# Kernel optimization log

Measured on AMD Instinct MI355X. Metric: run time of the kernel, lower is better.

Reference implementation:

```python
import jax, jax.numpy as jnp
import numpy as np

DIM = 128
NUM_HEADS = 16
DPH = DIM // NUM_HEADS
N_ATOMS = 50000
N_EDGES = 400000
LN_EPS = 1e-5


def setup_inputs() -> dict:
    key = jax.random.key(0)
    ks = jax.random.split(key, 12)
    inp = {
        "node_feat": jax.random.normal(ks[0], (N_ATOMS, DIM), jnp.float32),
        "edge_feat": jax.random.normal(ks[1], (N_EDGES, NUM_HEADS, DPH), jnp.float32),
        "edge_vec": jax.random.normal(ks[2], (N_EDGES, 3, 1, 1), jnp.float32),
        "radial": jax.random.uniform(ks[3], (N_EDGES,), jnp.float32),
        "qkv_w": jax.random.normal(ks[4], (DIM, 3 * DIM), jnp.float32) / np.sqrt(DIM),
        "qkv_b": jnp.zeros((3 * DIM,), jnp.float32),
        "out_w": jax.random.normal(ks[5], (DIM, DIM), jnp.float32) / np.sqrt(DIM),
        "out_b": jnp.zeros((DIM,), jnp.float32),
        "ln_g": jnp.ones((DIM,), jnp.float32),
        "ln_b": jnp.zeros((DIM,), jnp.float32),
        "row": jax.random.randint(ks[6], (N_EDGES,), 0, N_ATOMS, jnp.int32),
        "col": jax.random.randint(ks[7], (N_EDGES,), 0, N_ATOMS, jnp.int32),
        "natoms": N_ATOMS,
    }
    return inp


def _layer_norm(x, g, b):
    mu = jnp.mean(x, axis=-1, keepdims=True)
    var = jnp.mean(jnp.square(x - mu), axis=-1, keepdims=True)
    return (x - mu) * jax.lax.rsqrt(var + LN_EPS) * g + b


def reference(node_feat, edge_feat, edge_vec, radial, qkv_w, qkv_b, out_w, out_b,
              ln_g, ln_b, row, col, natoms):
    # LayerNorm + QKV projection (dense)
    h = _layer_norm(node_feat, ln_g, ln_b)                     # [N, D]
    qkv = h @ qkv_w + qkv_b                                    # [N, 3D]
    qkv = qkv.reshape(-1, NUM_HEADS, 3 * DPH)                  # [N, H, 3*Dh]
    q, k, v = qkv[..., :DPH], qkv[..., DPH:2 * DPH], qkv[..., 2 * DPH:]
    # Gather by edge indices
    q_row, k_col, v_col = q[row], k[col], v[col]               # [E, H, Dh]
    # Per-edge attention (exact erf GELU, matching torch nn.GELU default)
    attn = jax.nn.gelu(jnp.sum(q_row * k_col, axis=-1), approximate=False)
    attn = attn * radial[:, None]                              # [E, H]
    # Scalar message + scatter-add
    m_feat = v_col * edge_feat * attn[..., None]               # [E, H, Dh]
    m_feat = jax.ops.segment_sum(m_feat, row, num_segments=natoms)
    m_feat = m_feat.reshape(natoms, DIM)                       # [N, D]
    # Vector message + scatter-add
    m_vec = v_col[:, None, :, :] * edge_vec                    # [E, 3, H, Dh]
    m_vec = jax.ops.segment_sum(m_vec, row, num_segments=natoms)
    delta_node_vec = m_vec.reshape(natoms, 3, DIM)             # [N, 3, D]
    delta_node_feat = m_feat @ out_w + out_b                   # [N, D]
    return delta_node_feat, delta_node_vec
```

## Files before the change

### kernel.cpp

```cpp
#include <hip/hip_runtime.h>
#include <math.h>

#define DIM 128
#define NHEADS 16
#define DPH 8
#define NATOMS 50000
#define NEDGES 400000
#define LN_EPS 1e-5f

typedef float f32x4 __attribute__((ext_vector_type(4)));
typedef short s16x8 __attribute__((ext_vector_type(8)));

static __device__ __forceinline__ unsigned short f2bf(float f) {
  unsigned u = __builtin_bit_cast(unsigned, f);
  unsigned r = (u + 0x7FFFu + ((u >> 16) & 1u)) >> 16;
  return (unsigned short)r;
}
static __device__ __forceinline__ unsigned packbf(float lo, float hi) {
  return (unsigned)f2bf(lo) | ((unsigned)f2bf(hi) << 16);
}
static __device__ __forceinline__ float bflo(unsigned u) {
  return __builtin_bit_cast(float, u << 16);
}
static __device__ __forceinline__ float bfhi(unsigned u) {
  return __builtin_bit_cast(float, u & 0xffff0000u);
}

static __device__ __forceinline__ float gelu_fast(float x) {
  const float c0 = 0.7978845608028654f;
  const float c1 = 0.044715f;
  float u = c0 * (x + c1 * x * x * x);
  return __fdividef(x, 1.0f + __expf(-2.0f * u));
}

#define HIST_NB ((NEDGES + 255) / 256)
#define SCAN_NB 196
#define LN_NB (NATOMS / 16)

__global__ __launch_bounds__(256) void k_convert(
    const float* __restrict__ qkv_w, const float* __restrict__ out_w,
    unsigned short* __restrict__ wTq, unsigned short* __restrict__ wTo)
{
  const int idx = blockIdx.x * 256 + threadIdx.x;
  if (idx < 384 * 128) {
    const int c = idx >> 7, k = idx & 127;
    wTq[idx] = f2bf(qkv_w[k * 384 + c]);
  } else {
    const int i2 = idx - 384 * 128;
    const int c = i2 >> 7, k = i2 & 127;
    wTo[i2] = f2bf(out_w[k * 128 + c]);
  }
}

__global__ __launch_bounds__(256) void k_ln_qkv_hist(
    const float* __restrict__ node, const unsigned short* __restrict__ wTq,
    const float* __restrict__ bias, const float* __restrict__ g,
    const float* __restrict__ beta, unsigned* __restrict__ qb,
    unsigned* __restrict__ kvb, const int* __restrict__ row,
    int* __restrict__ cnt)
{
  if (blockIdx.x >= LN_NB) {
    const int e = (blockIdx.x - LN_NB) * 256 + threadIdx.x;
    if (e < NEDGES) atomicAdd(&cnt[row[e]], 1);
    return;
  }

  __shared__ float hpad[16][132];
  __shared__ float so[16][388];
  const int a0 = blockIdx.x * 16;
  const int tid = threadIdx.x;
  const int wid = tid >> 6;
  const int lane = tid & 63;

  for (int j = 0; j < 4; ++j) {
    const int a = wid * 4 + j;
    const float x0 = node[(size_t)(a0 + a) * DIM + lane];
    const float x1 = node[(size_t)(a0 + a) * DIM + 64 + lane];
    float s = x0 + x1;
    #pragma unroll
    for (int m = 1; m < 64; m <<= 1) s += __shfl_xor(s, m);
    const float mu = s * (1.0f / 128.0f);
    const float d0 = x0 - mu, d1 = x1 - mu;
    float v = d0 * d0 + d1 * d1;
    #pragma unroll
    for (int m = 1; m < 64; m <<= 1) v += __shfl_xor(v, m);
    const float rs = rsqrtf(v * (1.0f / 128.0f) + LN_EPS);
    hpad[a][lane]      = d0 * rs * g[lane]      + beta[lane];
    hpad[a][64 + lane] = d1 * rs * g[64 + lane] + beta[64 + lane];
  }
  __syncthreads();

  const int lrow = lane & 15;
  const int lquad = lane >> 4;
  const int colbase = wid * 96;

  s16x8 afrag[4];
  #pragma unroll
  for (int ks = 0; ks < 4; ++ks) {
    const int koff = ks * 32 + lquad * 8;
    const float4 p0 = *reinterpret_cast<const float4*>(&hpad[lrow][koff]);
    const float4 p1 = *reinterpret_cast<const float4*>(&hpad[lrow][koff + 4]);
    s16x8 af;
    af[0] = (short)f2bf(p0.x); af[1] = (short)f2bf(p0.y);
    af[2] = (short)f2bf(p0.z); af[3] = (short)f2bf(p0.w);
    af[4] = (short)f2bf(p1.x); af[5] = (short)f2bf(p1.y);
    af[6] = (short)f2bf(p1.z); af[7] = (short)f2bf(p1.w);
    afrag[ks] = af;
  }

  f32x4 acc[6];
  #pragma unroll
  for (int tt = 0; tt < 6; ++tt) acc[tt] = (f32x4){0.f, 0.f, 0.f, 0.f};

  #pragma unroll
  for (int tt = 0; tt < 6; ++tt) {
    const int cg = colbase + tt * 16 + lrow;
    #pragma unroll
    for (int ks = 0; ks < 4; ++ks) {
      const s16x8 bf = *reinterpret_cast<const s16x8*>(
          &wTq[(size_t)cg * 128 + ks * 32 + lquad * 8]);
      acc[tt] = __builtin_amdgcn_mfma_f32_16x16x32_bf16(afrag[ks], bf, acc[tt], 0, 0, 0);
    }
  }

  #pragma unroll
  for (int tt = 0; tt < 6; ++tt) {
    const int cg = colbase + tt * 16 + lrow;
    const float bz = bias[cg];
    const int hj = cg / 24;
    const int off = cg - hj * 24;
    int moff;
    if (off < 8)       moff = hj * 8 + off;
    else if (off < 16) moff = 128 + (hj * 8 + off - 8) * 2;
    else               moff = 128 + (hj * 8 + off - 16) * 2 + 1;
    #pragma unroll
    for (int r = 0; r < 4; ++r)
      so[lquad * 4 + r][moff] = acc[tt][r] + bz;
  }
  __syncthreads();

  #pragma unroll
  for (int kk = 0; kk < 4; ++kk) {
    const int i = tid + kk * 256;
    const int rowi = i >> 6;
    const int c2 = i & 63;
    qb[(size_t)(a0 + rowi) * 64 + c2] =
        packbf(so[rowi][2 * c2], so[rowi][2 * c2 + 1]);
  }
  #pragma unroll
  for (int kk = 0; kk < 8; ++kk) {
    const int i = tid + kk * 256;
    const int rowi = i >> 7;
    const int c = i & 127;
    kvb[(size_t)(a0 + rowi) * 128 + c] =
        packbf(so[rowi][128 + 2 * c], so[rowi][128 + 2 * c + 1]);
  }
}

__global__ __launch_bounds__(256) void k_scan1(const int* __restrict__ cnt,
                                               int* __restrict__ locx,
                                               int* __restrict__ psum) {
  __shared__ int sh[256];
  const int tid = threadIdx.x;
  const int i = blockIdx.x * 256 + tid;
  const int v = (i < NATOMS) ? cnt[i] : 0;
  sh[tid] = v;
  __syncthreads();
  #pragma unroll
  for (int off = 1; off < 256; off <<= 1) {
    const int cur = sh[tid];
    const int add = (tid >= off) ? sh[tid - off] : 0;
    __syncthreads();
    sh[tid] = cur + add;
    __syncthreads();
  }
  if (i < NATOMS) locx[i] = sh[tid] - v;
  if (tid == 255) psum[blockIdx.x] = sh[255];
}

__global__ __launch_bounds__(256) void k_scan23(const int* __restrict__ psum,
                                                const int* __restrict__ locx,
                                                int* __restrict__ base,
                                                int* __restrict__ cursor) {
  __shared__ int ws[4];
  const int bid = blockIdx.x;
  const int tid = threadIdx.x;
  const int lane = tid & 63;
  const int wid = tid >> 6;

  int s = (tid < bid) ? psum[tid] : 0;
  #pragma unroll
  for (int m = 1; m < 64; m <<= 1) s += __shfl_xor(s, m);
  if (lane == 0) ws[wid] = s;
  __syncthreads();
  const int off = ws[0] + ws[1] + ws[2] + ws[3];

  const int i = bid * 256 + tid;
  if (i < NATOMS) {
    const int b = locx[i] + off;
    base[i] = b;
    cursor[i] = b;
  }
  if (bid == 0 && tid == 0) base[NATOMS] = NEDGES;
}

__global__ __launch_bounds__(256) void k_scatter(
    const int* __restrict__ row, const int* __restrict__ col,
    const float* __restrict__ radial, const float* __restrict__ evec,
    int* __restrict__ cursor, int4* __restrict__ descA,
    float2* __restrict__ descB)
{
  const int e = blockIdx.x * 256 + threadIdx.x;
  if (e < NEDGES) {
    const int p = atomicAdd(&cursor[row[e]], 1);
    descA[p] = make_int4(e, col[e], __float_as_int(radial[e]),
                         __float_as_int(evec[(size_t)e * 3]));
    descB[p] = make_float2(evec[(size_t)e * 3 + 1], evec[(size_t)e * 3 + 2]);
  }
}

__global__ __launch_bounds__(256) void k_edge_csr(
    const unsigned* __restrict__ qb, const uint2* __restrict__ kvb,
    const float2* __restrict__ ef2, const int4* __restrict__ descA,
    const float2* __restrict__ descB, const int* __restrict__ base,
    unsigned* __restrict__ mfeatw, float* __restrict__ outvec)
{
  const int tid = threadIdx.x;
  const int a = blockIdx.x * 4 + (tid >> 6);
  const int t = tid & 63;

  const int pBeg = __builtin_amdgcn_readfirstlane(base[a]);
  const int pEnd = __builtin_amdgcn_readfirstlane(base[a + 1]);

  float f0 = 0.f, f1 = 0.f;
  float va0 = 0.f, va1 = 0.f, vb0 = 0.f, vb1 = 0.f, vc0 = 0.f, vc1 = 0.f;

  if (pBeg < pEnd) {
    const unsigned qp = qb[(size_t)a * 64 + t];
    const float q0 = bflo(qp), q1 = bfhi(qp);
    const int pLast = pEnd - 1;

    int4 u0, u1, u2, u3;
    float2 w0, w1, w2, w3;
    uint2 kvA0, kvA1, kvA2, kvA3, kvB0, kvB1, kvB2, kvB3;
    float2 efA0, efA1, efA2, efA3, efB0, efB1, efB2, efB3;
    float rA0, rA1, rA2, rA3, xA0, xA1, xA2, xA3;
    float yA0, yA1, yA2, yA3, zA0, zA1, zA2, zA3;
    float rB0, rB1, rB2, rB3, xB0, xB1, xB2, xB3;
    float yB0, yB1, yB2, yB3, zB0, zB1, zB2, zB3;

#define LOAD_DESC(P) do {                                                   \
    const int j0_ = ((P)     <= pLast) ? (P)     : pLast;                   \
    const int j1_ = ((P) + 1 <= pLast) ? (P) + 1 : pLast;                   \
    const int j2_ = ((P) + 2 <= pLast) ? (P) + 2 : pLast;                   \
    const int j3_ = ((P) + 3 <= pLast) ? (P) + 3 : pLast;                   \
    u0 = descA[j0_]; w0 = descB[j0_];                                       \
    u1 = descA[j1_]; w1 = descB[j1_];                                       \
    u2 = descA[j2_]; w2 = descB[j2_];                                       \
    u3 = descA[j3_]; w3 = descB[j3_];                                       \
  } while (0)

#define COPY_PAY(S) do {                                                    \
    r##S##0 = __int_as_float(u0.z); x##S##0 = __int_as_float(u0.w);         \
    y##S##0 = w0.x; z##S##0 = w0.y;                                         \
    r##S##1 = __int_as_float(u1.z); x##S##1 = __int_as_float(u1.w);         \
    y##S##1 = w1.x; z##S##1 = w1.y;                                         \
    r##S##2 = __int_as_float(u2.z); x##S##2 = __int_as_float(u2.w);         \
    y##S##2 = w2.x; z##S##2 = w2.y;                                         \
    r##S##3 = __int_as_float(u3.z); x##S##3 = __int_as_float(u3.w);         \
    y##S##3 = w3.x; z##S##3 = w3.y;                                         \
  } while (0)

#define ISSUE_DATA(S) do {                                                  \
    kv##S##0 = kvb[(size_t)(unsigned)u0.y * 64 + t];                        \
    ef##S##0 = ef2[(size_t)(unsigned)u0.x * 64 + t];                        \
    kv##S##1 = kvb[(size_t)(unsigned)u1.y * 64 + t];                        \
    ef##S##1 = ef2[(size_t)(unsigned)u1.x * 64 + t];                        \
    kv##S##2 = kvb[(size_t)(unsigned)u2.y * 64 + t];                        \
    ef##S##2 = ef2[(size_t)(unsigned)u2.x * 64 + t];                        \
    kv##S##3 = kvb[(size_t)(unsigned)u3.y * 64 + t];                        \
    ef##S##3 = ef2[(size_t)(unsigned)u3.x * 64 + t];                        \
  } while (0)

#define EDGE1(KV, EF, RR, XX, YY, ZZ, MM) do {                              \
    const float kx0_ = bflo(KV.x), kx1_ = bflo(KV.y);                       \
    const float vx0_ = bfhi(KV.x) * (MM), vx1_ = bfhi(KV.y) * (MM);         \
    float pd_ = q0 * kx0_; pd_ = fmaf(q1, kx1_, pd_);                       \
    pd_ += __shfl_xor(pd_, 1); pd_ += __shfl_xor(pd_, 2);                   \
    const float at_ = gelu_fast(pd_) * (RR);                                \
    f0 = fmaf(vx0_ * EF.x, at_, f0);                                        \
    f1 = fmaf(vx1_ * EF.y, at_, f1);                                        \
    va0 = fmaf(vx0_, (XX), va0); va1 = fmaf(vx1_, (XX), va1);               \
    vb0 = fmaf(vx0_, (YY), vb0); vb1 = fmaf(vx1_, (YY), vb1);               \
    vc0 = fmaf(vx0_, (ZZ), vc0); vc1 = fmaf(vx1_, (ZZ), vc1);               \
  } while (0)

#define COMPUTE(S, P) do {                                                  \
    const float m1_ = ((P) + 1 < pEnd) ? 1.f : 0.f;                         \
    const float m2_ = ((P) + 2 < pEnd) ? 1.f : 0.f;                         \
    const float m3_ = ((P) + 3 < pEnd) ? 1.f : 0.f;                         \
    EDGE1(kv##S##0, ef##S##0, r##S##0, x##S##0, y##S##0, z##S##0, 1.f);     \
    EDGE1(kv##S##1, ef##S##1, r##S##1, x##S##1, y##S##1, z##S##1, m1_);     \
    EDGE1(kv##S##2, ef##S##2, r##S##2, x##S##2, y##S##2, z##S##2, m2_);     \
    EDGE1(kv##S##3, ef##S##3, r##S##3, x##S##3, y##S##3, z##S##3, m3_);     \
  } while (0)

    LOAD_DESC(pBeg);
    COPY_PAY(A); ISSUE_DATA(A);
    LOAD_DESC(pBeg + 4);
    COPY_PAY(B); ISSUE_DATA(B);
    LOAD_DESC(pBeg + 8);

    int p = pBeg;
    while (true) {
      COMPUTE(A, p);
      p += 4; if (p >= pEnd) break;
      COPY_PAY(A); ISSUE_DATA(A);
      LOAD_DESC(p + 8);
      COMPUTE(B, p);
      p += 4; if (p >= pEnd) break;
      COPY_PAY(B); ISSUE_DATA(B);
      LOAD_DESC(p + 8);
    }

#undef LOAD_DESC
#undef COPY_PAY
#undef ISSUE_DATA
#undef EDGE1
#undef COMPUTE
  }

  mfeatw[(size_t)a * 64 + t] = packbf(f0, f1);
  float* ov = outvec + (size_t)a * 384 + 2 * t;
  *reinterpret_cast<float2*>(ov)       = make_float2(va0, va1);
  *reinterpret_cast<float2*>(ov + 128) = make_float2(vb0, vb1);
  *reinterpret_cast<float2*>(ov + 256) = make_float2(vc0, vc1);
}

__global__ __launch_bounds__(256) void k_out(
    const unsigned short* __restrict__ mfeatb,
    const unsigned short* __restrict__ wTo,
    const float* __restrict__ bias, float* __restrict__ out)
{
  __shared__ float so[16][132];
  const int a0 = blockIdx.x * 16;
  const int tid = threadIdx.x;
  const int wid = tid >> 6;
  const int lane = tid & 63;
  const int lrow = lane & 15;
  const int lquad = lane >> 4;

  s16x8 afrag[4];
  #pragma unroll
  for (int ks = 0; ks < 4; ++ks)
    afrag[ks] = *reinterpret_cast<const s16x8*>(
        &mfeatb[(size_t)(a0 + lrow) * 128 + ks * 32 + lquad * 8]);

  f32x4 acc[2];
  acc[0] = (f32x4){0.f, 0.f, 0.f, 0.f};
  acc[1] = (f32x4){0.f, 0.f, 0.f, 0.f};

  #pragma unroll
  for (int tt = 0; tt < 2; ++tt) {
    const int cg = wid * 32 + tt * 16 + lrow;
    #pragma unroll
    for (int ks = 0; ks < 4; ++ks) {
      const s16x8 bf = *reinterpret_cast<const s16x8*>(
          &wTo[(size_t)cg * 128 + ks * 32 + lquad * 8]);
      acc[tt] = __builtin_amdgcn_mfma_f32_16x16x32_bf16(afrag[ks], bf, acc[tt], 0, 0, 0);
    }
  }

  #pragma unroll
  for (int tt = 0; tt < 2; ++tt) {
    const int cg = wid * 32 + tt * 16 + lrow;
    const float bz = bias[cg];
    #pragma unroll
    for (int r = 0; r < 4; ++r)
      so[lquad * 4 + r][cg] = acc[tt][r] + bz;
  }
  __syncthreads();

  f32x4* out4 = (f32x4*)out;
  #pragma unroll
  for (int kk = 0; kk < 2; ++kk) {
    const int idx4 = tid + kk * 256;
    const int rowi = idx4 >> 5;
    const int c4 = idx4 & 31;
    out4[(size_t)(a0 + rowi) * 32 + c4] =
        *reinterpret_cast<const f32x4*>(&so[rowi][c4 * 4]);
  }
}

extern "C" void kernel_launch(void* const* d_in, const int* in_sizes, int n_in,
                              void* d_out, int out_size, void* d_ws, size_t ws_size,
                              hipStream_t stream) {
  const float* node_feat = (const float*)d_in[0];
  const float* edge_feat = (const float*)d_in[1];
  const float* edge_vec  = (const float*)d_in[2];
  const float* radial    = (const float*)d_in[3];
  const float* qkv_w     = (const float*)d_in[4];
  const float* qkv_b     = (const float*)d_in[5];
  const float* out_w     = (const float*)d_in[6];
  const float* out_b     = (const float*)d_in[7];
  const float* ln_g      = (const float*)d_in[8];
  const float* ln_b      = (const float*)d_in[9];
  const int*   row       = (const int*)d_in[10];
  const int*   col       = (const int*)d_in[11];

  float* out      = (float*)d_out;
  float* out_feat = out;
  float* out_vec  = out + (size_t)NATOMS * DIM;

  unsigned* qb  = (unsigned*)d_ws;
  unsigned* kvb = qb + (size_t)NATOMS * 64;
  unsigned short* mfeatb = (unsigned short*)(kvb + (size_t)NATOMS * 128);
  unsigned short* wTq = mfeatb + (size_t)NATOMS * 128;
  unsigned short* wTo = wTq + 384 * 128;
  int4* descA  = (int4*)(wTo + 128 * 128);
  float2* descB = (float2*)(descA + NEDGES);
  int* cnt    = (int*)(descB + NEDGES);
  int* base   = cnt + NATOMS;
  int* cursor = base + NATOMS + 1;
  int* locx   = cursor + NATOMS;
  int* psum   = locx + NATOMS;

  hipMemsetAsync(cnt, 0, NATOMS * sizeof(int), stream);

  k_convert<<<256, 256, 0, stream>>>(qkv_w, out_w, wTq, wTo);

  k_ln_qkv_hist<<<LN_NB + HIST_NB, 256, 0, stream>>>(
      node_feat, wTq, qkv_b, ln_g, ln_b, qb, kvb, row, cnt);

  k_scan1<<<SCAN_NB, 256, 0, stream>>>(cnt, locx, psum);
  k_scan23<<<SCAN_NB, 256, 0, stream>>>(psum, locx, base, cursor);
  k_scatter<<<HIST_NB, 256, 0, stream>>>(row, col, radial, edge_vec, cursor,
                                         descA, descB);

  k_edge_csr<<<(NATOMS / 4), 256, 0, stream>>>(
      qb, (const uint2*)kvb, (const float2*)edge_feat, descA, descB, base,
      (unsigned*)mfeatb, out_vec);

  k_out<<<NATOMS / 16, 256, 0, stream>>>(mfeatb, wTo, out_b, out_feat);
}
```

Before: 210.7 us.

## Remap edge kernel to one head per lane, four atoms per wavefront

```diff
diff --git a/kernel.cpp b/kernel.cpp
--- a/kernel.cpp
+++ b/kernel.cpp
@@ -39,9 +39,11 @@
 
 __global__ __launch_bounds__(256) void k_convert(
     const float* __restrict__ qkv_w, const float* __restrict__ out_w,
-    unsigned short* __restrict__ wTq, unsigned short* __restrict__ wTo)
+    unsigned short* __restrict__ wTq, unsigned short* __restrict__ wTo,
+    int* __restrict__ cnt)
 {
   const int idx = blockIdx.x * 256 + threadIdx.x;
+  if (idx < NATOMS) cnt[idx] = 0;
   if (idx < 384 * 128) {
     const int c = idx >> 7, k = idx & 127;
     wTq[idx] = f2bf(qkv_w[k * 384 + c]);
@@ -220,121 +222,126 @@
 }
 
 __global__ __launch_bounds__(256) void k_edge_csr(
-    const unsigned* __restrict__ qb, const uint2* __restrict__ kvb,
-    const float2* __restrict__ ef2, const int4* __restrict__ descA,
+    const uint4* __restrict__ qb4, const uint4* __restrict__ kvb4,
+    const float4* __restrict__ ef4, const int4* __restrict__ descA,
     const float2* __restrict__ descB, const int* __restrict__ base,
-    unsigned* __restrict__ mfeatw, float* __restrict__ outvec)
+    uint4* __restrict__ mfeat4, float* __restrict__ outvec)
 {
   const int tid = threadIdx.x;
-  const int a = blockIdx.x * 4 + (tid >> 6);
-  const int t = tid & 63;
-
-  const int pBeg = __builtin_amdgcn_readfirstlane(base[a]);
-  const int pEnd = __builtin_amdgcn_readfirstlane(base[a + 1]);
-
-  float f0 = 0.f, f1 = 0.f;
-  float va0 = 0.f, va1 = 0.f, vb0 = 0.f, vb1 = 0.f, vc0 = 0.f, vc1 = 0.f;
-
-  if (pBeg < pEnd) {
-    const unsigned qp = qb[(size_t)a * 64 + t];
-    const float q0 = bflo(qp), q1 = bfhi(qp);
-    const int pLast = pEnd - 1;
-
-    int4 u0, u1, u2, u3;
-    float2 w0, w1, w2, w3;
-    uint2 kvA0, kvA1, kvA2, kvA3, kvB0, kvB1, kvB2, kvB3;
-    float2 efA0, efA1, efA2, efA3, efB0, efB1, efB2, efB3;
-    float rA0, rA1, rA2, rA3, xA0, xA1, xA2, xA3;
-    float yA0, yA1, yA2, yA3, zA0, zA1, zA2, zA3;
-    float rB0, rB1, rB2, rB3, xB0, xB1, xB2, xB3;
-    float yB0, yB1, yB2, yB3, zB0, zB1, zB2, zB3;
-
-#define LOAD_DESC(P) do {                                                   \
-    const int j0_ = ((P)     <= pLast) ? (P)     : pLast;                   \
-    const int j1_ = ((P) + 1 <= pLast) ? (P) + 1 : pLast;                   \
-    const int j2_ = ((P) + 2 <= pLast) ? (P) + 2 : pLast;                   \
-    const int j3_ = ((P) + 3 <= pLast) ? (P) + 3 : pLast;                   \
-    u0 = descA[j0_]; w0 = descB[j0_];                                       \
-    u1 = descA[j1_]; w1 = descB[j1_];                                       \
-    u2 = descA[j2_]; w2 = descB[j2_];                                       \
-    u3 = descA[j3_]; w3 = descB[j3_];                                       \
+  const int lane = tid & 63;
+  const int sub = lane >> 4;
+  const int h = lane & 15;
+  const int a = (blockIdx.x * 4 + (tid >> 6)) * 4 + sub;
+
+  const int pBeg = base[a];
+  const int pEnd = base[a + 1];
+  const int deg = pEnd - pBeg;
+
+  int md = deg;
+  #pragma unroll
+  for (int m = 1; m < 64; m <<= 1) {
+    const int o = __shfl_xor(md, m);
+    md = md > o ? md : o;
+  }
+
+  float fa[8], vv0[8], vv1[8], vv2[8];
+  #pragma unroll
+  for (int i = 0; i < 8; ++i) { fa[i] = 0.f; vv0[i] = 0.f; vv1[i] = 0.f; vv2[i] = 0.f; }
+
+  if (md > 0) {
+    const int hi = (deg > 0) ? (pEnd - 1) : 0;
+
+    const uint4 qa = qb4[(size_t)a * 16 + h];
+    float q[8];
+    q[0] = bflo(qa.x); q[1] = bfhi(qa.x);
+    q[2] = bflo(qa.y); q[3] = bfhi(qa.y);
+    q[4] = bflo(qa.z); q[5] = bfhi(qa.z);
+    q[6] = bflo(qa.w); q[7] = bfhi(qa.w);
+
+    uint4 kv0A, kv1A, kv0B, kv1B;
+    float4 ef0A, ef1A, ef0B, ef1B;
+    int4 dA, dB;
+    float2 bA, bB;
+    float rA, xA, yA, zA, rB, xB, yB, zB;
+
+#define LDESC(D, BB, IT) do {                                               \
+    int pc_ = pBeg + (IT);                                                  \
+    pc_ = (pc_ <= hi) ? pc_ : hi;                                           \
+    D = descA[pc_];                                                         \
+    BB = descB[pc_];                                                        \
   } while (0)
 
-#define COPY_PAY(S) do {                                                    \
-    r##S##0 = __int_as_float(u0.z); x##S##0 = __int_as_float(u0.w);         \
-    y##S##0 = w0.x; z##S##0 = w0.y;                                         \
-    r##S##1 = __int_as_float(u1.z); x##S##1 = __int_as_float(u1.w);         \
-    y##S##1 = w1.x; z##S##1 = w1.y;                                         \
-    r##S##2 = __int_as_float(u2.z); x##S##2 = __int_as_float(u2.w);         \
-    y##S##2 = w2.x; z##S##2 = w2.y;                                         \
-    r##S##3 = __int_as_float(u3.z); x##S##3 = __int_as_float(u3.w);         \
-    y##S##3 = w3.x; z##S##3 = w3.y;                                         \
+#define STAGE(S, IT) do {                                                   \
+    const float m_ = ((IT) < deg) ? 1.f : 0.f;                              \
+    r##S = __int_as_float(d##S.z) * m_;                                     \
+    x##S = __int_as_float(d##S.w) * m_;                                     \
+    y##S = b##S.x * m_;                                                     \
+    z##S = b##S.y * m_;                                                     \
+    const size_t cb_ = (size_t)(unsigned)d##S.y * 32 + 2 * h;               \
+    const size_t eb_ = (size_t)(unsigned)d##S.x * 32 + 2 * h;               \
+    kv0##S = kvb4[cb_];                                                     \
+    kv1##S = kvb4[cb_ + 1];                                                 \
+    ef0##S = ef4[eb_];                                                      \
+    ef1##S = ef4[eb_ + 1];                                                  \
   } while (0)
 
-#define ISSUE_DATA(S) do {                                                  \
-    kv##S##0 = kvb[(size_t)(unsigned)u0.y * 64 + t];                        \
-    ef##S##0 = ef2[(size_t)(unsigned)u0.x * 64 + t];                        \
-    kv##S##1 = kvb[(size_t)(unsigned)u1.y * 64 + t];                        \
-    ef##S##1 = ef2[(size_t)(unsigned)u1.x * 64 + t];                        \
-    kv##S##2 = kvb[(size_t)(unsigned)u2.y * 64 + t];                        \
-    ef##S##2 = ef2[(size_t)(unsigned)u2.x * 64 + t];                        \
-    kv##S##3 = kvb[(size_t)(unsigned)u3.y * 64 + t];                        \
-    ef##S##3 = ef2[(size_t)(unsigned)u3.x * 64 + t];                        \
+#define COMPUTE(S) do {                                                     \
+    float k_[8], v_[8], e_[8];                                              \
+    k_[0] = bflo(kv0##S.x); v_[0] = bfhi(kv0##S.x);                         \
+    k_[1] = bflo(kv0##S.y); v_[1] = bfhi(kv0##S.y);                         \
+    k_[2] = bflo(kv0##S.z); v_[2] = bfhi(kv0##S.z);                         \
+    k_[3] = bflo(kv0##S.w); v_[3] = bfhi(kv0##S.w);                         \
+    k_[4] = bflo(kv1##S.x); v_[4] = bfhi(kv1##S.x);                         \
+    k_[5] = bflo(kv1##S.y); v_[5] = bfhi(kv1##S.y);                         \
+    k_[6] = bflo(kv1##S.z); v_[6] = bfhi(kv1##S.z);                         \
+    k_[7] = bflo(kv1##S.w); v_[7] = bfhi(kv1##S.w);                         \
+    e_[0] = ef0##S.x; e_[1] = ef0##S.y; e_[2] = ef0##S.z; e_[3] = ef0##S.w; \
+    e_[4] = ef1##S.x; e_[5] = ef1##S.y; e_[6] = ef1##S.z; e_[7] = ef1##S.w; \
+    float p_ = q[0] * k_[0];                                                \
+    p_ = fmaf(q[1], k_[1], p_); p_ = fmaf(q[2], k_[2], p_);                 \
+    p_ = fmaf(q[3], k_[3], p_); p_ = fmaf(q[4], k_[4], p_);                 \
+    p_ = fmaf(q[5], k_[5], p_); p_ = fmaf(q[6], k_[6], p_);                 \
+    p_ = fmaf(q[7], k_[7], p_);                                             \
+    const float at_ = gelu_fast(p_) * r##S;                                 \
+    _Pragma("unroll")                                                       \
+    for (int i_ = 0; i_ < 8; ++i_) {                                        \
+      fa[i_]  = fmaf(v_[i_] * e_[i_], at_, fa[i_]);                         \
+      vv0[i_] = fmaf(v_[i_], x##S, vv0[i_]);                                \
+      vv1[i_] = fmaf(v_[i_], y##S, vv1[i_]);                                \
+      vv2[i_] = fmaf(v_[i_], z##S, vv2[i_]);                                \
+    }                                                                       \
   } while (0)
 
-#define EDGE1(KV, EF, RR, XX, YY, ZZ, MM) do {                              \
-    const float kx0_ = bflo(KV.x), kx1_ = bflo(KV.y);                       \
-    const float vx0_ = bfhi(KV.x) * (MM), vx1_ = bfhi(KV.y) * (MM);         \
-    float pd_ = q0 * kx0_; pd_ = fmaf(q1, kx1_, pd_);                       \
-    pd_ += __shfl_xor(pd_, 1); pd_ += __shfl_xor(pd_, 2);                   \
-    const float at_ = gelu_fast(pd_) * (RR);                                \
-    f0 = fmaf(vx0_ * EF.x, at_, f0);                                        \
-    f1 = fmaf(vx1_ * EF.y, at_, f1);                                        \
-    va0 = fmaf(vx0_, (XX), va0); va1 = fmaf(vx1_, (XX), va1);               \
-    vb0 = fmaf(vx0_, (YY), vb0); vb1 = fmaf(vx1_, (YY), vb1);               \
-    vc0 = fmaf(vx0_, (ZZ), vc0); vc1 = fmaf(vx1_, (ZZ), vc1);               \
-  } while (0)
-
-#define COMPUTE(S, P) do {                                                  \
-    const float m1_ = ((P) + 1 < pEnd) ? 1.f : 0.f;                         \
-    const float m2_ = ((P) + 2 < pEnd) ? 1.f : 0.f;                         \
-    const float m3_ = ((P) + 3 < pEnd) ? 1.f : 0.f;                         \
-    EDGE1(kv##S##0, ef##S##0, r##S##0, x##S##0, y##S##0, z##S##0, 1.f);     \
-    EDGE1(kv##S##1, ef##S##1, r##S##1, x##S##1, y##S##1, z##S##1, m1_);     \
-    EDGE1(kv##S##2, ef##S##2, r##S##2, x##S##2, y##S##2, z##S##2, m2_);     \
-    EDGE1(kv##S##3, ef##S##3, r##S##3, x##S##3, y##S##3, z##S##3, m3_);     \
-  } while (0)
-
-    LOAD_DESC(pBeg);
-    COPY_PAY(A); ISSUE_DATA(A);
-    LOAD_DESC(pBeg + 4);
-    COPY_PAY(B); ISSUE_DATA(B);
-    LOAD_DESC(pBeg + 8);
-
-    int p = pBeg;
-    while (true) {
-      COMPUTE(A, p);
-      p += 4; if (p >= pEnd) break;
-      COPY_PAY(A); ISSUE_DATA(A);
-      LOAD_DESC(p + 8);
-      COMPUTE(B, p);
-      p += 4; if (p >= pEnd) break;
-      COPY_PAY(B); ISSUE_DATA(B);
-      LOAD_DESC(p + 8);
+    LDESC(dA, bA, 0);
+    LDESC(dB, bB, 1);
+    STAGE(A, 0);
+    STAGE(B, 1);
+    LDESC(dA, bA, 2);
+    LDESC(dB, bB, 3);
+
+    for (int it = 0; it < md; it += 2) {
+      COMPUTE(A);
+      if (it + 2 < md) { STAGE(A, it + 2); LDESC(dA, bA, it + 4); }
+      if (it + 1 >= md) break;
+      COMPUTE(B);
+      if (it + 3 < md) { STAGE(B, it + 3); LDESC(dB, bB, it + 5); }
     }
 
-#undef LOAD_DESC
-#undef COPY_PAY
-#undef ISSUE_DATA
-#undef EDGE1
+#undef LDESC
+#undef STAGE
 #undef COMPUTE
   }
 
-  mfeatw[(size_t)a * 64 + t] = packbf(f0, f1);
-  float* ov = outvec + (size_t)a * 384 + 2 * t;
-  *reinterpret_cast<float2*>(ov)       = make_float2(va0, va1);
-  *reinterpret_cast<float2*>(ov + 128) = make_float2(vb0, vb1);
-  *reinterpret_cast<float2*>(ov + 256) = make_float2(vc0, vc1);
+  mfeat4[(size_t)a * 16 + h] =
+      make_uint4(packbf(fa[0], fa[1]), packbf(fa[2], fa[3]),
+                 packbf(fa[4], fa[5]), packbf(fa[6], fa[7]));
+  float* ov = outvec + (size_t)a * 384 + 8 * h;
+  *reinterpret_cast<float4*>(ov)       = make_float4(vv0[0], vv0[1], vv0[2], vv0[3]);
+  *reinterpret_cast<float4*>(ov + 4)   = make_float4(vv0[4], vv0[5], vv0[6], vv0[7]);
+  *reinterpret_cast<float4*>(ov + 128) = make_float4(vv1[0], vv1[1], vv1[2], vv1[3]);
+  *reinterpret_cast<float4*>(ov + 132) = make_float4(vv1[4], vv1[5], vv1[6], vv1[7]);
+  *reinterpret_cast<float4*>(ov + 256) = make_float4(vv2[0], vv2[1], vv2[2], vv2[3]);
+  *reinterpret_cast<float4*>(ov + 260) = make_float4(vv2[4], vv2[5], vv2[6], vv2[7]);
 }
 
 __global__ __launch_bounds__(256) void k_out(
@@ -425,9 +432,7 @@
   int* locx   = cursor + NATOMS;
   int* psum   = locx + NATOMS;
 
-  hipMemsetAsync(cnt, 0, NATOMS * sizeof(int), stream);
-
-  k_convert<<<256, 256, 0, stream>>>(qkv_w, out_w, wTq, wTo);
+  k_convert<<<256, 256, 0, stream>>>(qkv_w, out_w, wTq, wTo, cnt);
 
   k_ln_qkv_hist<<<LN_NB + HIST_NB, 256, 0, stream>>>(
       node_feat, wTq, qkv_b, ln_g, ln_b, qb, kvb, row, cnt);
@@ -437,9 +442,9 @@
   k_scatter<<<HIST_NB, 256, 0, stream>>>(row, col, radial, edge_vec, cursor,
                                          descA, descB);
 
-  k_edge_csr<<<(NATOMS / 4), 256, 0, stream>>>(
-      qb, (const uint2*)kvb, (const float2*)edge_feat, descA, descB, base,
-      (unsigned*)mfeatb, out_vec);
+  k_edge_csr<<<NATOMS / 16, 256, 0, stream>>>(
+      (const uint4*)qb, (const uint4*)kvb, (const float4*)edge_feat,
+      descA, descB, base, (uint4*)mfeatb, out_vec);
 
   k_out<<<NATOMS / 16, 256, 0, stream>>>(mfeatb, wTo, out_b, out_feat);
 }
```

Result: slower. 224.5 us (+6.5%).
